# Kernel tuning notes

Measured on AMD Instinct MI355X. Metric: run time of the kernel, lower is better.

## Reference

```python
import jax, jax.numpy as jnp
import numpy as np

K_S = 2  # spatial order
K_T = 3  # temporal localization factor


def setup_inputs() -> dict:
    key = jax.random.key(0)
    ks = jax.random.split(key, 5)
    B, T, N = 8, 12, 250
    return {
        "history_data": jax.random.normal(ks[0], (B, T, N, 128), dtype=jnp.float32),
        "Prior": jax.random.normal(ks[1], (B, T, N, 64), dtype=jnp.float32),
        "Observed": jax.random.normal(ks[2], (B, T, N, 32), dtype=jnp.float32),
        "W_emb": jax.random.normal(ks[3], (224, 64), dtype=jnp.float32) * 0.05,
        "b_emb": jnp.zeros((64,), dtype=jnp.float32),
        "use_X": 1,
    }


def _transition(adj):
    # P = D^{-1} A : faithful to diag-embed @ adj, realized as row scaling
    rowsum = adj.sum(axis=-1) + 1e-9
    d_inv = 1.0 / rowsum
    d_inv = jnp.where(jnp.isinf(d_inv) | jnp.isnan(d_inv), 0.0, d_inv)
    return d_inv[..., :, None] * adj


def _forward(history_data, Prior, Observed, W_emb, b_emb):
    # nodevec: [B,T,N,64]
    nodevec = jnp.tanh(
        jnp.concatenate([history_data, Prior, Observed], axis=-1) @ W_emb + b_emb
    )
    # similarity: [B,T,N,N]
    sim = jax.nn.relu(jnp.einsum("btnd,btmd->btnm", nodevec, nodevec))
    # symmetric normalization D^{-1/2} S D^{-1/2}
    d = (sim.sum(axis=-1) + 1e-9) ** -0.5
    adj = d[..., :, None] * sim * d[..., None, :]
    P1 = jnp.swapaxes(_transition(adj), -2, -1)
    P2 = jnp.swapaxes(_transition(jnp.swapaxes(adj, -2, -1)), -2, -1)
    N = adj.shape[-1]
    mask = 1.0 - jnp.eye(N, dtype=adj.dtype)
    outs = []
    for g in (P1, P2):
        k1 = g
        ordered = [k1 * mask]
        for _k in range(2, K_S + 1):
            k1 = k1 @ g
            ordered.append(k1 * mask)
        for og in ordered:
            B, T, Nn, _ = og.shape
            # st_localization: tile each row K_T times along last dim
            ex = jnp.broadcast_to(og[..., None, :], (B, T, Nn, K_T, Nn))
            outs.append(ex.reshape(B, T, Nn, K_T * Nn))
    return tuple(outs)


def reference(history_data, Prior, Observed, W_emb, b_emb, use_X):
    # use_X == 1 path (fc_x_emb on concatenated features)
    return _forward(history_data, Prior, Observed, W_emb, b_emb)
```

## Files before the change

kernel.cpp:

```cpp
#include <hip/hip_runtime.h>
#include <hip/hip_bf16.h>

#define G_N 96
#define N_N 250
#define N_P 256
#define E_N 64
#define OUT_GSTRIDE (250 * 750)
#define OUT_STRIDE  (96 * 250 * 750)

typedef __attribute__((ext_vector_type(4))) float floatx4;
typedef __attribute__((ext_vector_type(2))) float floatx2;
typedef __attribute__((ext_vector_type(8))) short shortx8;
typedef __attribute__((ext_vector_type(4))) short shortx4;

__device__ __forceinline__ float bf2f(unsigned short u) {
    union { unsigned int i; float f; } v; v.i = ((unsigned int)u) << 16; return v.f;
}
__device__ __forceinline__ unsigned short f2bf(float f) {
    union { float f; unsigned int i; } v; v.f = f;
    unsigned int x = v.i;
    return (unsigned short)((x + 0x7fffu + ((x >> 16) & 1u)) >> 16);
}

__global__ __launch_bounds__(256) void k_embed(
    const float* __restrict__ hist, const float* __restrict__ prior,
    const float* __restrict__ obs, const float* __restrict__ Wemb,
    const float* __restrict__ bemb, unsigned short* __restrict__ nvb)
{
    __shared__ __attribute__((aligned(16))) float Xt[32][68];
    __shared__ __attribute__((aligned(16))) float Wl[32][64];
    const int t  = threadIdx.x;
    const int tx = t & 15, ty = t >> 4;
    const int rr0 = blockIdx.x * 64;
    const int g   = rr0 >> 8;
    const int n0  = rr0 & 255;

    float acc[4][4] = {};

    for (int c = 0; c < 7; ++c) {
        const float* src; int rowlen, off;
        if (c < 4)      { src = hist;  rowlen = 128; off = c << 5; }
        else if (c < 6) { src = prior; rowlen = 64;  off = (c - 4) << 5; }
        else            { src = obs;   rowlen = 32;  off = 0; }
        __syncthreads();
        {
            const int d  = t & 31;
            const int nb = t >> 5;
            #pragma unroll
            for (int p = 0; p < 8; ++p) {
                const int nl = nb + p * 8;
                const int n  = n0 + nl;
                float v = 0.0f;
                if (n < N_N) v = src[(size_t)(g * N_N + n) * rowlen + off + d];
                Xt[d][nl] = v;
            }
        }
        {
            const int e  = t & 63;
            const int db = t >> 6;
            #pragma unroll
            for (int p = 0; p < 8; ++p) {
                const int dl = db + p * 4;
                Wl[dl][e] = Wemb[(c * 32 + dl) * 64 + e];
            }
        }
        __syncthreads();
        #pragma unroll
        for (int k = 0; k < 32; ++k) {
            const float4 av = *(const float4*)&Xt[k][4 * ty];
            const float4 bv = *(const float4*)&Wl[k][4 * tx];
            const float a[4] = {av.x, av.y, av.z, av.w};
            const float b[4] = {bv.x, bv.y, bv.z, bv.w};
            #pragma unroll
            for (int r = 0; r < 4; ++r)
                #pragma unroll
                for (int cc = 0; cc < 4; ++cc)
                    acc[r][cc] = fmaf(a[r], b[cc], acc[r][cc]);
        }
    }
    #pragma unroll
    for (int r = 0; r < 4; ++r) {
        const int nl = 4 * ty + r;
        const int n  = n0 + nl;
        unsigned short* d2 = nvb + ((size_t)g * N_P + (n0 + nl)) * E_N + 4 * tx;
        #pragma unroll
        for (int cc = 0; cc < 4; ++cc) {
            float v = 0.0f;
            if (n < N_N) v = tanhf(acc[r][cc] + bemb[4 * tx + cc]);
            d2[cc] = f2bf(v);
        }
    }
}

__global__ __launch_bounds__(256) void k_sim(
    const unsigned short* __restrict__ nvb, unsigned short* __restrict__ Sb,
    float* __restrict__ rowsum)
{
    const int blk = blockIdx.x;
    const int g   = blk >> 4;
    const int i0  = (blk & 15) << 4;
    const int t    = threadIdx.x;
    const int w    = t >> 6;
    const int lane = t & 63;
    const int m = lane & 15, kg = lane >> 4;

    const shortx8* nvg = (const shortx8*)(nvb + (size_t)g * N_P * E_N);
    const shortx8 a0 = nvg[(i0 + m) * 8 + kg];
    const shortx8 a1 = nvg[(i0 + m) * 8 + 4 + kg];

    floatx4 acc[4];
    const floatx4 zero = {0.f, 0.f, 0.f, 0.f};
    #pragma unroll
    for (int tt = 0; tt < 4; ++tt) {
        const int j = (w << 6) + (tt << 4) + m;
        const shortx8 b0 = nvg[j * 8 + kg];
        const shortx8 b1 = nvg[j * 8 + 4 + kg];
        floatx4 c = zero;
        c = __builtin_amdgcn_mfma_f32_16x16x32_bf16(a0, b0, c, 0, 0, 0);
        c = __builtin_amdgcn_mfma_f32_16x16x32_bf16(a1, b1, c, 0, 0, 0);
        acc[tt] = c;
    }

    float v[4] = {0.f, 0.f, 0.f, 0.f};
    unsigned short* Sg = Sb + (size_t)g * N_P * N_P;
    #pragma unroll
    for (int tt = 0; tt < 4; ++tt) {
        #pragma unroll
        for (int r = 0; r < 4; ++r) {
            float s = acc[tt][r];
            s = s > 0.f ? s : 0.f;
            const int il = (kg << 2) + r;
            const int j  = (w << 6) + (tt << 4) + m;
            Sg[(size_t)(i0 + il) * N_P + j] = f2bf(s);
            v[r] += s;
        }
    }
    #pragma unroll
    for (int r = 0; r < 4; ++r) {
        v[r] += __shfl_xor(v[r], 1);
        v[r] += __shfl_xor(v[r], 2);
        v[r] += __shfl_xor(v[r], 4);
        v[r] += __shfl_xor(v[r], 8);
    }
    __shared__ float rs[4][16];
    if (m == 0) {
        #pragma unroll
        for (int r = 0; r < 4; ++r) rs[w][(kg << 2) + r] = v[r];
    }
    __syncthreads();
    if (t < 16) rowsum[g * N_P + i0 + t] = rs[0][t] + rs[1][t] + rs[2][t] + rs[3][t];
}

__global__ __launch_bounds__(256) void k_trans(
    const unsigned short* __restrict__ Sb, const float* __restrict__ rowsum,
    float* __restrict__ cArr, float* __restrict__ wArr)
{
    const int blk = (blockIdx.x & 7) * 768 + (blockIdx.x >> 3);
    const int g  = blk >> 6;
    const int r0 = (blk & 63) << 2;
    const int t = threadIdx.x;
    const int w = t >> 6, lane = t & 63;
    __shared__ __attribute__((aligned(16))) float dL[N_P];
    dL[t] = rsqrtf(rowsum[g * N_P + t] + 1e-9f);
    __syncthreads();
    const int row = r0 + w;
    const shortx4 sv = *(const shortx4*)(Sb + (size_t)g * N_P * N_P
                                         + (size_t)row * N_P + lane * 4);
    const float4 dv = *(const float4*)&dL[lane * 4];
    float a = bf2f((unsigned short)sv[0]) * dv.x
            + bf2f((unsigned short)sv[1]) * dv.y
            + bf2f((unsigned short)sv[2]) * dv.z
            + bf2f((unsigned short)sv[3]) * dv.w;
    #pragma unroll
    for (int s = 32; s; s >>= 1) a += __shfl_xor(a, s);
    if (lane == 0) {
        const float d = dL[row];
        const float r = 1.0f / (d * a + 1e-9f);
        const float c = r * d;
        cArr[g * N_P + row] = c;
        wArr[g * N_P + row] = c * d;
    }
}

__global__ __launch_bounds__(256) void k_pq(
    const unsigned short* __restrict__ Sb, const float* __restrict__ rowsum,
    const float* __restrict__ cArr, const float* __restrict__ wArr,
    float* __restrict__ out)
{
    const int blk = (blockIdx.x & 7) * 192 + (blockIdx.x >> 3);
    const int g   = blk >> 4;
    const int i0  = (blk & 15) << 4;
    const int t    = threadIdx.x;
    const int w    = t >> 6;
    const int lane = t & 63;
    const int m = lane & 15, kg = lane >> 4;

    __shared__ __attribute__((aligned(16))) unsigned short As[16][40];
    __shared__ __attribute__((aligned(16))) unsigned short Bs[256][40];
    __shared__ __attribute__((aligned(16))) float wL[N_P];
    __shared__ __attribute__((aligned(16))) float cC[N_P];
    __shared__ float dR16[16];
    __shared__ __attribute__((aligned(16))) float pAll[16][260];
    __shared__ __attribute__((aligned(16))) float qAll[16][260];

    wL[t] = wArr[g * N_P + t];
    cC[t] = cArr[g * N_P + t];
    if (t < 16) dR16[t] = rsqrtf(rowsum[g * N_P + i0 + t] + 1e-9f);

    const unsigned short* Sg = Sb + (size_t)g * N_P * N_P;

    floatx4 acc[4];
    const floatx4 zero = {0.f, 0.f, 0.f, 0.f};
    #pragma unroll
    for (int tt = 0; tt < 4; ++tt) acc[tt] = zero;

    for (int kb = 0; kb < 8; ++kb) {
        __syncthreads();
        if (t < 64) {
            const int row = t >> 2, c4 = t & 3;
            *(uint4*)&As[row][c4 * 8] =
                *(const uint4*)(Sg + (size_t)(i0 + row) * N_P + kb * 32 + c4 * 8);
        }
        #pragma unroll
        for (int q4 = 0; q4 < 4; ++q4) {
            const int u = t + (q4 << 8);
            const int row = u >> 2, c4 = u & 3;
            *(uint4*)&Bs[row][c4 * 8] =
                *(const uint4*)(Sg + (size_t)row * N_P + kb * 32 + c4 * 8);
        }
        __syncthreads();
        #pragma unroll
        for (int q2 = 0; q2 < 2; ++q2) {
            const int idx = t + (q2 << 8);
            const int row = idx >> 5, kl = idx & 31;
            const int col = kb * 32 + kl;
            float pv = dR16[row] * bf2f(As[row][kl]) * cC[col];
            if (i0 + row == col) pv = 0.f;
            pAll[row][col] = pv;
        }
        const shortx8 a = *(const shortx8*)&As[m][kg << 3];
        const float4 w0 = *(const float4*)&wL[kb * 32 + (kg << 3)];
        const float4 w1 = *(const float4*)&wL[kb * 32 + (kg << 3) + 4];
        const float wv[8] = {w0.x, w0.y, w0.z, w0.w, w1.x, w1.y, w1.z, w1.w};
        shortx8 aw;
        #pragma unroll
        for (int u = 0; u < 8; ++u)
            aw[u] = (short)f2bf(bf2f((unsigned short)a[u]) * wv[u]);
        #pragma unroll
        for (int tt = 0; tt < 4; ++tt) {
            const shortx8 b = *(const shortx8*)&Bs[(w << 6) + (tt << 4) + m][kg << 3];
            acc[tt] = __builtin_amdgcn_mfma_f32_16x16x32_bf16(aw, b, acc[tt], 0, 0, 0);
        }
    }

    #pragma unroll
    for (int tt = 0; tt < 4; ++tt) {
        #pragma unroll
        for (int r = 0; r < 4; ++r) {
            const int lrow = (kg << 2) + r;
            const int col  = (w << 6) + (tt << 4) + m;
            float qv = acc[tt][r] * dR16[lrow] * cC[col];
            if (i0 + lrow == col) qv = 0.f;
            qAll[lrow][col] = qv;
        }
    }
    __syncthreads();

    for (int rr = 0; rr < 4; ++rr) {
        const int row = (rr << 2) + w;
        const int i   = i0 + row;
        if (i >= N_N) continue;
        const floatx4 p4 = *(const floatx4*)&pAll[row][lane << 2];
        const floatx4 q4 = *(const floatx4*)&qAll[row][lane << 2];
        if (lane >= 63) continue;
        const floatx2 pxy = {p4[0], p4[1]}, pzw = {p4[2], p4[3]};
        const floatx2 qxy = {q4[0], q4[1]}, qzw = {q4[2], q4[3]};
        float* b0 = out + (size_t)g * OUT_GSTRIDE + (size_t)i * 750 + (lane << 2);
        float* b1 = b0 + (size_t)OUT_STRIDE;
        float* b2 = b0 + 2 * (size_t)OUT_STRIDE;
        float* b3 = b0 + 3 * (size_t)OUT_STRIDE;
        #pragma unroll
        for (int rep = 0; rep < 3; ++rep) {
            const int o = rep * 250;
            *(floatx2*)(b0 + o) = pxy;
            *(floatx2*)(b1 + o) = qxy;
            *(floatx2*)(b2 + o) = pxy;
            *(floatx2*)(b3 + o) = qxy;
            if (lane < 62) {
                *(floatx2*)(b0 + o + 2) = pzw;
                *(floatx2*)(b1 + o + 2) = qzw;
                *(floatx2*)(b2 + o + 2) = pzw;
                *(floatx2*)(b3 + o + 2) = qzw;
            }
        }
    }
}

extern "C" void kernel_launch(void* const* d_in, const int* in_sizes, int n_in,
                              void* d_out, int out_size, void* d_ws, size_t ws_size,
                              hipStream_t stream) {
    const float* hist  = (const float*)d_in[0];
    const float* prior = (const float*)d_in[1];
    const float* obs   = (const float*)d_in[2];
    const float* Wemb  = (const float*)d_in[3];
    const float* bemb  = (const float*)d_in[4];
    float* out = (float*)d_out;

    char* p = (char*)d_ws;
    unsigned short* nvb = (unsigned short*)p; p += (size_t)G_N * N_P * E_N * 2;
    unsigned short* Sb  = (unsigned short*)p; p += (size_t)G_N * N_P * N_P * 2;
    float* rowsum = (float*)p; p += (size_t)G_N * N_P * 4;
    float* cArr   = (float*)p; p += (size_t)G_N * N_P * 4;
    float* wArr   = (float*)p; p += (size_t)G_N * N_P * 4;

    k_embed<<<dim3(G_N * N_P / 64), dim3(256), 0, stream>>>(hist, prior, obs, Wemb, bemb, nvb);
    k_sim  <<<dim3(G_N * 16),       dim3(256), 0, stream>>>(nvb, Sb, rowsum);
    k_trans<<<dim3(G_N * 64),       dim3(256), 0, stream>>>(Sb, rowsum, cArr, wArr);
    k_pq   <<<dim3(G_N * 16),       dim3(256), 0, stream>>>(Sb, rowsum, cArr, wArr, out);
}
```

Measured before the change: 369.9 us.

## Stream P output directly from global memory and interleave its stores with the MFMA loop

The P-tile output is now computed straight from the bf16 similarity rows in global memory and written out, instead of being staged through a shared-memory buffer inside the k-loop. Odd blocks write P before the matmul and even blocks after, so that store traffic from some blocks overlaps compute in others. The change also remaps block indices in k_embed and k_sim with an XCD-style swizzle for locality. The shared-memory footprint shrinks, at the cost of an extra global read of S rows and an added barrier.

```diff
diff --git a/kernel.cpp b/kernel.cpp
--- a/kernel.cpp
+++ b/kernel.cpp
@@ -31,7 +31,8 @@
     __shared__ __attribute__((aligned(16))) float Wl[32][64];
     const int t  = threadIdx.x;
     const int tx = t & 15, ty = t >> 4;
-    const int rr0 = blockIdx.x * 64;
+    const int b   = (blockIdx.x & 7) * 48 + (blockIdx.x >> 3);
+    const int rr0 = b * 64;
     const int g   = rr0 >> 8;
     const int n0  = rr0 & 255;
 
@@ -70,12 +71,12 @@
             const float4 av = *(const float4*)&Xt[k][4 * ty];
             const float4 bv = *(const float4*)&Wl[k][4 * tx];
             const float a[4] = {av.x, av.y, av.z, av.w};
-            const float b[4] = {bv.x, bv.y, bv.z, bv.w};
+            const float b2[4] = {bv.x, bv.y, bv.z, bv.w};
             #pragma unroll
             for (int r = 0; r < 4; ++r)
                 #pragma unroll
                 for (int cc = 0; cc < 4; ++cc)
-                    acc[r][cc] = fmaf(a[r], b[cc], acc[r][cc]);
+                    acc[r][cc] = fmaf(a[r], b2[cc], acc[r][cc]);
         }
     }
     #pragma unroll
@@ -96,7 +97,7 @@
     const unsigned short* __restrict__ nvb, unsigned short* __restrict__ Sb,
     float* __restrict__ rowsum)
 {
-    const int blk = blockIdx.x;
+    const int blk = (blockIdx.x & 7) * 192 + (blockIdx.x >> 3);
     const int g   = blk >> 4;
     const int i0  = (blk & 15) << 4;
     const int t    = threadIdx.x;
@@ -200,14 +201,52 @@
     __shared__ __attribute__((aligned(16))) float wL[N_P];
     __shared__ __attribute__((aligned(16))) float cC[N_P];
     __shared__ float dR16[16];
-    __shared__ __attribute__((aligned(16))) float pAll[16][260];
     __shared__ __attribute__((aligned(16))) float qAll[16][260];
 
     wL[t] = wArr[g * N_P + t];
     cC[t] = cArr[g * N_P + t];
     if (t < 16) dR16[t] = rsqrtf(rowsum[g * N_P + i0 + t] + 1e-9f);
+    __syncthreads();
 
     const unsigned short* Sg = Sb + (size_t)g * N_P * N_P;
+    float* o0 = out + (size_t)g * OUT_GSTRIDE;
+    float* o1 = o0 + (size_t)OUT_STRIDE;
+    float* o2 = o0 + 2 * (size_t)OUT_STRIDE;
+    float* o3 = o0 + 3 * (size_t)OUT_STRIDE;
+    const int c0 = lane << 2;
+
+    auto writeP = [&]() {
+        if (c0 >= 252) return;
+        #pragma unroll
+        for (int rr = 0; rr < 4; ++rr) {
+            const int row = (rr << 2) + w;
+            const int i   = i0 + row;
+            if (i >= N_N) continue;
+            const float dI = dR16[row];
+            const shortx4 sv = *(const shortx4*)(Sg + (size_t)i * N_P + c0);
+            const float4 cc4 = *(const float4*)&cC[c0];
+            const float p0 = (i == c0)     ? 0.f : dI * bf2f((unsigned short)sv[0]) * cc4.x;
+            const float p1 = (i == c0 + 1) ? 0.f : dI * bf2f((unsigned short)sv[1]) * cc4.y;
+            const float p2 = (i == c0 + 2) ? 0.f : dI * bf2f((unsigned short)sv[2]) * cc4.z;
+            const float p3 = (i == c0 + 3) ? 0.f : dI * bf2f((unsigned short)sv[3]) * cc4.w;
+            const floatx2 pxy = {p0, p1}, pzw = {p2, p3};
+            float* b0 = o0 + (size_t)i * 750 + c0;
+            float* b2 = o2 + (size_t)i * 750 + c0;
+            #pragma unroll
+            for (int rep = 0; rep < 3; ++rep) {
+                const int o = rep * 250;
+                *(floatx2*)(b0 + o) = pxy;
+                *(floatx2*)(b2 + o) = pxy;
+                if (lane < 62) {
+                    *(floatx2*)(b0 + o + 2) = pzw;
+                    *(floatx2*)(b2 + o + 2) = pzw;
+                }
+            }
+        }
+    };
+
+    const bool pfirst = (blk & 1) != 0;
+    if (pfirst) writeP();
 
     floatx4 acc[4];
     const floatx4 zero = {0.f, 0.f, 0.f, 0.f};
@@ -229,15 +268,6 @@
                 *(const uint4*)(Sg + (size_t)row * N_P + kb * 32 + c4 * 8);
         }
         __syncthreads();
-        #pragma unroll
-        for (int q2 = 0; q2 < 2; ++q2) {
-            const int idx = t + (q2 << 8);
-            const int row = idx >> 5, kl = idx & 31;
-            const int col = kb * 32 + kl;
-            float pv = dR16[row] * bf2f(As[row][kl]) * cC[col];
-            if (i0 + row == col) pv = 0.f;
-            pAll[row][col] = pv;
-        }
         const shortx8 a = *(const shortx8*)&As[m][kg << 3];
         const float4 w0 = *(const float4*)&wL[kb * 32 + (kg << 3)];
         const float4 w1 = *(const float4*)&wL[kb * 32 + (kg << 3) + 4];
@@ -266,34 +296,29 @@
     }
     __syncthreads();
 
+    #pragma unroll
     for (int rr = 0; rr < 4; ++rr) {
         const int row = (rr << 2) + w;
         const int i   = i0 + row;
         if (i >= N_N) continue;
-        const floatx4 p4 = *(const floatx4*)&pAll[row][lane << 2];
-        const floatx4 q4 = *(const floatx4*)&qAll[row][lane << 2];
-        if (lane >= 63) continue;
-        const floatx2 pxy = {p4[0], p4[1]}, pzw = {p4[2], p4[3]};
+        const floatx4 q4 = *(const floatx4*)&qAll[row][c0];
+        if (c0 >= 252) continue;
         const floatx2 qxy = {q4[0], q4[1]}, qzw = {q4[2], q4[3]};
-        float* b0 = out + (size_t)g * OUT_GSTRIDE + (size_t)i * 750 + (lane << 2);
-        float* b1 = b0 + (size_t)OUT_STRIDE;
-        float* b2 = b0 + 2 * (size_t)OUT_STRIDE;
-        float* b3 = b0 + 3 * (size_t)OUT_STRIDE;
+        float* b1 = o1 + (size_t)i * 750 + c0;
+        float* b3 = o3 + (size_t)i * 750 + c0;
         #pragma unroll
         for (int rep = 0; rep < 3; ++rep) {
             const int o = rep * 250;
-            *(floatx2*)(b0 + o) = pxy;
             *(floatx2*)(b1 + o) = qxy;
-            *(floatx2*)(b2 + o) = pxy;
             *(floatx2*)(b3 + o) = qxy;
             if (lane < 62) {
-                *(floatx2*)(b0 + o + 2) = pzw;
                 *(floatx2*)(b1 + o + 2) = qzw;
-                *(floatx2*)(b2 + o + 2) = pzw;
                 *(floatx2*)(b3 + o + 2) = qzw;
             }
         }
     }
+
+    if (!pfirst) writeP();
 }
 
 extern "C" void kernel_launch(void* const* d_in, const int* in_sizes, int n_in,
```

New measurement: 363.4 us (median of 2 runs). Within noise of the previous version (-1.8%).
